# Performance work log

Measured on AMD Instinct MI355X. Metric: run time of the kernel, lower is better.

Reference implementation:

```python
import jax, jax.numpy as jnp
import numpy as np

NEG_SLOPE = 0.2  # PyG GATConv default negative_slope


def _gat_conv(h, src, dst, N, W, a_src, a_dst, b, heads):
    """PyG GATConv (eval mode, self-loops already in src/dst).
    h: [N, F_in], W: [F_in, heads*C], a_src/a_dst: [heads, C], b: [heads*C]."""
    C = W.shape[1] // heads
    hl = (h @ W).reshape(N, heads, C)                      # [N,H,C]
    al_s = jnp.einsum('nhc,hc->nh', hl, a_src)             # [N,H]
    al_d = jnp.einsum('nhc,hc->nh', hl, a_dst)             # [N,H]
    e = jax.nn.leaky_relu(al_s[src] + al_d[dst], NEG_SLOPE)  # [E,H]
    # segment softmax over incoming edges of each destination node
    m = jax.ops.segment_max(e, dst, num_segments=N)        # [N,H]
    ex = jnp.exp(e - m[dst])
    s = jax.ops.segment_sum(ex, dst, num_segments=N)
    alpha = ex / (s[dst] + 1e-16)                          # [E,H]
    out = jax.ops.segment_sum(hl[src] * alpha[:, :, None], dst, num_segments=N)
    return out.reshape(N, heads * C) + b


def setup_inputs() -> dict:
    key = jax.random.key(0)
    ks = jax.random.split(key, 16)
    N, E, D = 30000, 240000, 64
    NUM_ENT, NUM_REL, NUM_DRUGS = 100000, 64, 200
    sc = 0.1
    return {
        'x': jax.random.randint(ks[0], (N,), 0, NUM_ENT),
        'edge_index': jax.random.randint(ks[1], (2, E), 0, N),
        'edge_type': jax.random.randint(ks[2], (N,), 0, NUM_REL),
        'ent_emb': jax.random.normal(ks[3], (NUM_ENT, D), jnp.float32) * sc,
        'rel_emb': jax.random.normal(ks[4], (NUM_REL, D), jnp.float32) * sc,
        'W1': jax.random.normal(ks[5], (2 * D, 8 * D), jnp.float32) * sc,
        'att1_src': jax.random.normal(ks[6], (8, D), jnp.float32) * sc,
        'att1_dst': jax.random.normal(ks[7], (8, D), jnp.float32) * sc,
        'b1': jax.random.normal(ks[8], (8 * D,), jnp.float32) * sc,
        'W2': jax.random.normal(ks[9], (9 * D, D), jnp.float32) * sc,
        'att2_src': jax.random.normal(ks[10], (1, D), jnp.float32) * sc,
        'att2_dst': jax.random.normal(ks[11], (1, D), jnp.float32) * sc,
        'b2': jax.random.normal(ks[12], (D,), jnp.float32) * sc,
        'fc_w': jax.random.normal(ks[13], (D, NUM_DRUGS), jnp.float32) * sc,
        'fc_b': jax.random.normal(ks[14], (NUM_DRUGS,), jnp.float32) * sc,
    }


def reference(x, edge_index, edge_type, ent_emb, rel_emb, W1, att1_src, att1_dst, b1,
              W2, att2_src, att2_dst, b2, fc_w, fc_b):
    N = x.shape[0]
    loop = jnp.arange(N)
    src = jnp.concatenate([edge_index[0], loop])  # GATConv add_self_loops=True
    dst = jnp.concatenate([edge_index[1], loop])
    ent = ent_emb[x]                               # [N,D]
    rel = rel_emb[edge_type]                       # [N,D]
    h = jnp.concatenate([ent, rel], axis=-1)       # [N,2D]  (dropout is identity in eval)
    h = jax.nn.elu(_gat_conv(h, src, dst, N, W1, att1_src, att1_dst, b1, heads=8))  # [N,8D]
    h = jnp.concatenate([h, ent], axis=-1)         # [N,9D]
    h = jax.nn.elu(_gat_conv(h, src, dst, N, W2, att2_src, att2_dst, b2, heads=1))  # [N,D]
    g = jnp.mean(h, axis=0, keepdims=True)         # [1,D]
    return g @ fc_w + fc_b                         # [1,num_drugs]
```

## Files before the change

### kernel.cpp

```cpp
#include <hip/hip_runtime.h>
#include <math.h>

#define NEG_SLOPE 0.2f

typedef __attribute__((ext_vector_type(8))) short short8;
typedef __attribute__((ext_vector_type(4))) float f32x4;
typedef __attribute__((ext_vector_type(2))) float f32x2;

__device__ __forceinline__ float lrelu(float v) { return v > 0.f ? v : NEG_SLOPE * v; }
__device__ __forceinline__ float elu(float v) { return v > 0.f ? v : (__expf(v) - 1.f); }
__device__ __forceinline__ unsigned short f2b(float f) {
    unsigned u = __float_as_uint(f);
    return (unsigned short)((u + 0x7FFFu + ((u >> 16) & 1u)) >> 16);
}
__device__ __forceinline__ unsigned packb(float a, float b) {
    return ((unsigned)f2b(b) << 16) | (unsigned)f2b(a);
}
__device__ __forceinline__ unsigned short pack8(float a, float b) {
    return (unsigned short)(__builtin_amdgcn_cvt_pk_fp8_f32(a, b, 0, false) & 0xFFFF);
}
__device__ __forceinline__ f32x2 unpack8(unsigned v) {
    return __builtin_amdgcn_cvt_pk_f32_fp8((int)v, false);
}
__device__ __forceinline__ f32x2 unpack8hi(unsigned v) {
    return __builtin_amdgcn_cvt_pk_f32_fp8((int)v, true);
}
__device__ __forceinline__ unsigned bpack_trunc(f32x2 f) {
    return (__float_as_uint(f.y) & 0xFFFF0000u) | (__float_as_uint(f.x) >> 16);
}
__device__ __forceinline__ int sw(int r, int o) { return (o ^ (r & 7)) << 3; }

__global__ void prep_k(const int* __restrict__ x, const int* __restrict__ et,
                       const int* __restrict__ ei,
                       const float* __restrict__ ent_emb, const float* __restrict__ rel_emb,
                       const float* __restrict__ W1, const float* __restrict__ W2,
                       unsigned* __restrict__ h1b2, unsigned short* __restrict__ W1t,
                       unsigned short* __restrict__ W2t, unsigned char* __restrict__ h2q8,
                       int* __restrict__ deg, int N, int E) {
    int t = blockIdx.x * blockDim.x + threadIdx.x;
    if (t < N * 64) {
        int n = t >> 6, j = t & 63;
        float v0, v1;
        if (j < 32) {
            const float* e = ent_emb + (size_t)x[n] * 64 + 2 * j;
            v0 = e[0]; v1 = e[1];
            *(unsigned short*)(h2q8 + (size_t)n * 576 + 512 + 2 * j) = pack8(v0, v1);
        } else {
            const float* r = rel_emb + (size_t)et[n] * 64 + 2 * (j - 32);
            v0 = r[0]; v1 = r[1];
        }
        h1b2[t] = packb(v0, v1);
    }
    if (t < 512 * 128) {
        int n = t >> 7, kk = t & 127;
        W1t[t] = f2b(W1[(size_t)kk * 512 + n]);
    }
    if (t < 64 * 576) {
        int n = t / 576, k = t % 576;
        W2t[t] = f2b(W2[(size_t)k * 64 + n]);
    }
    if (t < E + N) {
        int dst = t < E ? ei[E + t] : t - E;
        atomicAdd(&deg[dst], 1);
    }
}

__global__ __launch_bounds__(256) void scan_k(const int* __restrict__ deg,
                                              int* __restrict__ offs,
                                              int* __restrict__ bstate,
                                              int N, int Etot, int NB) {
    __shared__ int s[256];
    __shared__ int sbase;
    int b = blockIdx.x, t = threadIdx.x;
    int i = b * 256 + t;
    int v = (i < N) ? deg[i] : 0;
    s[t] = v;
    __syncthreads();
    for (int off = 1; off < 256; off <<= 1) {
        int tmp = (t >= off) ? s[t - off] : 0;
        __syncthreads();
        s[t] += tmp;
        __syncthreads();
    }
    int total = s[255];
    if (t == 0) {
        if (b == 0) {
            atomicExch(&bstate[0], (total << 2) | 2);
            sbase = 0;
        } else {
            atomicExch(&bstate[b], (total << 2) | 1);
            int run = 0;
            for (int p = b - 1; p >= 0;) {
                int stv;
                do { stv = atomicAdd(&bstate[p], 0); } while ((stv & 3) == 0);
                run += (stv >> 2);
                if ((stv & 3) == 2) break;
                p--;
            }
            atomicExch(&bstate[b], ((run + total) << 2) | 2);
            sbase = run;
        }
    }
    __syncthreads();
    if (i < N) offs[i] = sbase + s[t] - v;
    if (b == NB - 1 && t == 0) offs[N] = Etot;
}

__global__ __launch_bounds__(256) void fillgemm1_k(const int* __restrict__ ei, int E, int N,
                                                   const int* __restrict__ offs,
                                                   int* __restrict__ cursor,
                                                   int* __restrict__ csr,
                                                   const unsigned short* __restrict__ A,
                                                   const unsigned short* __restrict__ W1t,
                                                   const float* __restrict__ a1s,
                                                   const float* __restrict__ a1d,
                                                   unsigned char* __restrict__ hl8,
                                                   float* __restrict__ als,
                                                   float* __restrict__ ald,
                                                   int FB, int NMB) {
    __shared__ __align__(16) unsigned short As[128 * 128];
    __shared__ __align__(16) unsigned short Bs[64 * 128];
    int bid = blockIdx.x;
    int tid = threadIdx.x;
    if (bid < FB) {
        int e = bid * 256 + tid;
        if (e < E + N) {
            int src = e < E ? ei[e] : e - E;
            int dst = e < E ? ei[E + e] : e - E;
            int pos = offs[dst] + atomicAdd(&cursor[dst], 1);
            csr[pos] = src;
        }
        return;
    }
    int g = bid - FB;
    int h = g / NMB, mb = g - h * NMB;
    int m0 = mb * 128;
    int M = N;
    for (int c = tid; c < 2048; c += 256) {
        int r = c >> 4, o = c & 15;
        int gr = m0 + r;
        uint4 v = make_uint4(0u, 0u, 0u, 0u);
        if (gr < M) v = *(const uint4*)(A + (size_t)gr * 128 + o * 8);
        *(uint4*)(As + r * 128 + sw(r, o)) = v;
    }
    for (int c = tid; c < 1024; c += 256) {
        int r = c >> 4, o = c & 15;
        uint4 v = *(const uint4*)(W1t + (size_t)(h * 64 + r) * 128 + o * 8);
        *(uint4*)(Bs + r * 128 + sw(r, o)) = v;
    }
    __syncthreads();
    int w = tid >> 6, lane = tid & 63;
    int wr = w * 32;
    int m16 = lane & 15, quad = lane >> 4;
    f32x4 acc[2][4] = {};
#pragma unroll
    for (int kk = 0; kk < 128; kk += 32) {
        int ob = (kk >> 3) + quad;
        short8 b[4];
#pragma unroll
        for (int j = 0; j < 4; j++) {
            int r = j * 16 + m16;
            b[j] = *(const short8*)(Bs + r * 128 + sw(r, ob));
        }
#pragma unroll
        for (int i = 0; i < 2; i++) {
            int r = wr + i * 16 + m16;
            short8 a = *(const short8*)(As + r * 128 + sw(r, ob));
#pragma unroll
            for (int j = 0; j < 4; j++)
                acc[i][j] = __builtin_amdgcn_mfma_f32_16x16x32_bf16(a, b[j], acc[i][j], 0, 0, 0);
        }
    }
#pragma unroll
    for (int i = 0; i < 2; i++)
#pragma unroll
        for (int j = 0; j < 4; j++)
#pragma unroll
            for (int reg = 0; reg < 4; reg++) {
                int row = m0 + wr + i * 16 + quad * 4 + reg;
                int col = h * 64 + j * 16 + m16;
                if (row < M)
                    hl8[(size_t)row * 512 + col] =
                        (unsigned char)(__builtin_amdgcn_cvt_pk_fp8_f32(acc[i][j][reg] * 8.f,
                                                                        0.f, 0, false) & 0xFF);
            }
    float sa[2][4] = {}, sd[2][4] = {};
#pragma unroll
    for (int j = 0; j < 4; j++) {
        int col = h * 64 + j * 16 + m16;
        float ws_ = a1s[col], wd_ = a1d[col];
#pragma unroll
        for (int i = 0; i < 2; i++)
#pragma unroll
            for (int reg = 0; reg < 4; reg++) {
                sa[i][reg] += acc[i][j][reg] * ws_;
                sd[i][reg] += acc[i][j][reg] * wd_;
            }
    }
#pragma unroll
    for (int m = 1; m < 16; m <<= 1)
#pragma unroll
        for (int i = 0; i < 2; i++)
#pragma unroll
            for (int reg = 0; reg < 4; reg++) {
                sa[i][reg] += __shfl_xor(sa[i][reg], m, 64);
                sd[i][reg] += __shfl_xor(sd[i][reg], m, 64);
            }
    if (m16 == 0)
#pragma unroll
        for (int i = 0; i < 2; i++)
#pragma unroll
            for (int reg = 0; reg < 4; reg++) {
                int row = m0 + wr + i * 16 + quad * 4 + reg;
                if (row < M) { als[row * 8 + h] = sa[i][reg]; ald[row * 8 + h] = sd[i][reg]; }
            }
}

#define ACCP(e_, u_)                                      \
    {                                                     \
        f32x2 g0 = unpack8(u_.x), g1 = unpack8hi(u_.x);   \
        f32x2 g2 = unpack8(u_.y), g3 = unpack8hi(u_.y);   \
        acc[0] += (e_) * g0.x; acc[1] += (e_) * g0.y;     \
        acc[2] += (e_) * g1.x; acc[3] += (e_) * g1.y;     \
        acc[4] += (e_) * g2.x; acc[5] += (e_) * g2.y;     \
        acc[6] += (e_) * g3.x; acc[7] += (e_) * g3.y;     \
    }

__global__ __launch_bounds__(256) void agg1_k(const unsigned char* __restrict__ hl8,
                                              const float* __restrict__ als1,
                                              const float* __restrict__ ald1,
                                              const float* __restrict__ b1,
                                              const int* __restrict__ offs,
                                              const int* __restrict__ csr,
                                              unsigned char* __restrict__ h2q8, int N) {
    int wv = threadIdx.x >> 6;
    int t = threadIdx.x & 63;
    int n = blockIdx.x * 4 + wv;
    if (n >= N) return;
    int h = t >> 3;
    float dl = ald1[n * 8 + h];
    int p0 = offs[n], p1 = offs[n + 1];
    float acc[8] = {};
    float ssum = 0.f;
    int p = p0;
    for (; p + 4 <= p1; p += 4) {
        int sA = csr[p], sB = csr[p + 1], sC = csr[p + 2], sD = csr[p + 3];
        float eA = __expf(lrelu(als1[sA * 8 + h] + dl));
        float eB = __expf(lrelu(als1[sB * 8 + h] + dl));
        float eC = __expf(lrelu(als1[sC * 8 + h] + dl));
        float eD = __expf(lrelu(als1[sD * 8 + h] + dl));
        uint2 vA = *(const uint2*)(hl8 + (size_t)sA * 512 + t * 8);
        uint2 vB = *(const uint2*)(hl8 + (size_t)sB * 512 + t * 8);
        uint2 vC = *(const uint2*)(hl8 + (size_t)sC * 512 + t * 8);
        uint2 vD = *(const uint2*)(hl8 + (size_t)sD * 512 + t * 8);
        ssum += (eA + eB) + (eC + eD);
        ACCP(eA, vA);
        ACCP(eB, vB);
        ACCP(eC, vC);
        ACCP(eD, vD);
    }
    for (; p < p1; p++) {
        int sA = csr[p];
        float eA = __expf(lrelu(als1[sA * 8 + h] + dl));
        uint2 vA = *(const uint2*)(hl8 + (size_t)sA * 512 + t * 8);
        ssum += eA;
        ACCP(eA, vA);
    }
    float iv = 0.125f / (ssum + 1e-16f);
    float4 bq0 = *(const float4*)(b1 + t * 8);
    float4 bq1 = *(const float4*)(b1 + t * 8 + 4);
    float r0 = elu(acc[0] * iv + bq0.x);
    float r1 = elu(acc[1] * iv + bq0.y);
    float r2 = elu(acc[2] * iv + bq0.z);
    float r3 = elu(acc[3] * iv + bq0.w);
    float r4 = elu(acc[4] * iv + bq1.x);
    float r5 = elu(acc[5] * iv + bq1.y);
    float r6 = elu(acc[6] * iv + bq1.z);
    float r7 = elu(acc[7] * iv + bq1.w);
    uint2 o;
    int d0 = __builtin_amdgcn_cvt_pk_fp8_f32(r0, r1, 0, false);
    o.x = (unsigned)__builtin_amdgcn_cvt_pk_fp8_f32(r2, r3, d0, true);
    int d1 = __builtin_amdgcn_cvt_pk_fp8_f32(r4, r5, 0, false);
    o.y = (unsigned)__builtin_amdgcn_cvt_pk_fp8_f32(r6, r7, d1, true);
    *(uint2*)(h2q8 + (size_t)n * 576 + t * 8) = o;
}

__global__ __launch_bounds__(256) void gemm2_k(const unsigned char* __restrict__ Aq8,
                                               const unsigned short* __restrict__ Bt,
                                               const float* __restrict__ a2s,
                                               const float* __restrict__ a2d,
                                               unsigned char* __restrict__ hl2q,
                                               float* __restrict__ als2,
                                               float* __restrict__ ald2, int M) {
    __shared__ __align__(16) unsigned short As[64 * 64];
    __shared__ __align__(16) unsigned short Bs[64 * 64];
    int tid = threadIdx.x;
    int m0 = blockIdx.x * 64;
    int w = tid >> 6, lane = tid & 63;
    int m16 = lane & 15, quad = lane >> 4;
    f32x4 acc[4] = {};
    for (int k0 = 0; k0 < 576; k0 += 64) {
        __syncthreads();
        {
            int r = tid >> 2, o = tid & 3;
            int gr = m0 + r;
            uint4 v = make_uint4(0u, 0u, 0u, 0u);
            if (gr < M) v = *(const uint4*)(Aq8 + (size_t)gr * 576 + k0 + o * 16);
            uint4 w0, w1;
            w0.x = bpack_trunc(unpack8(v.x));   w0.y = bpack_trunc(unpack8hi(v.x));
            w0.z = bpack_trunc(unpack8(v.y));   w0.w = bpack_trunc(unpack8hi(v.y));
            w1.x = bpack_trunc(unpack8(v.z));   w1.y = bpack_trunc(unpack8hi(v.z));
            w1.z = bpack_trunc(unpack8(v.w));   w1.w = bpack_trunc(unpack8hi(v.w));
            *(uint4*)(As + r * 64 + sw(r, 2 * o)) = w0;
            *(uint4*)(As + r * 64 + sw(r, 2 * o + 1)) = w1;
        }
        for (int c = tid; c < 512; c += 256) {
            int r = c >> 3, o = c & 7;
            uint4 v = *(const uint4*)(Bt + (size_t)r * 576 + k0 + o * 8);
            *(uint4*)(Bs + r * 64 + sw(r, o)) = v;
        }
        __syncthreads();
#pragma unroll
        for (int kk = 0; kk < 64; kk += 32) {
            int ob = (kk >> 3) + quad;
            int r = w * 16 + m16;
            short8 a = *(const short8*)(As + r * 64 + sw(r, ob));
#pragma unroll
            for (int j = 0; j < 4; j++) {
                int rb = j * 16 + m16;
                short8 b = *(const short8*)(Bs + rb * 64 + sw(rb, ob));
                acc[j] = __builtin_amdgcn_mfma_f32_16x16x32_bf16(a, b, acc[j], 0, 0, 0);
            }
        }
    }
#pragma unroll
    for (int j = 0; j < 4; j++)
#pragma unroll
        for (int reg = 0; reg < 4; reg++) {
            int row = m0 + w * 16 + quad * 4 + reg;
            int col = j * 16 + m16;
            if (row < M)
                hl2q[(size_t)row * 64 + col] =
                    (unsigned char)(__builtin_amdgcn_cvt_pk_fp8_f32(acc[j][reg], 0.f, 0, false) & 0xFF);
        }
    float sa[4] = {}, sd[4] = {};
#pragma unroll
    for (int j = 0; j < 4; j++) {
        int col = j * 16 + m16;
        float as_ = a2s[col], ad_ = a2d[col];
#pragma unroll
        for (int reg = 0; reg < 4; reg++) {
            sa[reg] += acc[j][reg] * as_;
            sd[reg] += acc[j][reg] * ad_;
        }
    }
#pragma unroll
    for (int m = 1; m < 16; m <<= 1)
#pragma unroll
        for (int reg = 0; reg < 4; reg++) {
            sa[reg] += __shfl_xor(sa[reg], m, 64);
            sd[reg] += __shfl_xor(sd[reg], m, 64);
        }
    if (m16 == 0)
#pragma unroll
        for (int reg = 0; reg < 4; reg++) {
            int row = m0 + w * 16 + quad * 4 + reg;
            if (row < M) { als2[row] = sa[reg]; ald2[row] = sd[reg]; }
        }
}

__global__ __launch_bounds__(256) void agg2_k(const unsigned short* __restrict__ hl2q16,
                                              const float* __restrict__ als2,
                                              const float* __restrict__ ald2,
                                              const float* __restrict__ b2,
                                              const int* __restrict__ offs,
                                              const int* __restrict__ csr,
                                              float* __restrict__ gpart, int N) {
    __shared__ float red[512];
    int slot = threadIdx.x >> 5, l = threadIdx.x & 31;
    int n = blockIdx.x * 8 + slot;
    float v0 = 0.f, v1 = 0.f;
    if (n < N) {
        float dl = ald2[n];
        int p0 = offs[n], p1 = offs[n + 1];
        float a0 = 0.f, a1 = 0.f, ssum = 0.f;
        int p = p0;
        for (; p + 1 < p1; p += 2) {
            int sA = csr[p], sB = csr[p + 1];
            float lA = als2[sA], lB = als2[sB];
            unsigned hA = hl2q16[sA * 32 + l];
            unsigned hB = hl2q16[sB * 32 + l];
            float xA = __expf(lrelu(lA + dl));
            float xB = __expf(lrelu(lB + dl));
            ssum += xA + xB;
            f32x2 fA = unpack8(hA), fB = unpack8(hB);
            a0 += xA * fA.x + xB * fB.x;
            a1 += xA * fA.y + xB * fB.y;
        }
        if (p < p1) {
            int sA = csr[p];
            float xA = __expf(lrelu(als2[sA] + dl));
            ssum += xA;
            f32x2 fA = unpack8(hl2q16[sA * 32 + l]);
            a0 += xA * fA.x;
            a1 += xA * fA.y;
        }
        float inv = 1.f / (ssum + 1e-16f);
        v0 = elu(a0 * inv + b2[2 * l]);
        v1 = elu(a1 * inv + b2[2 * l + 1]);
    }
    red[slot * 64 + 2 * l] = v0;
    red[slot * 64 + 2 * l + 1] = v1;
    __syncthreads();
    if (threadIdx.x < 64) {
        float s = 0.f;
#pragma unroll
        for (int ss = 0; ss < 8; ss++) s += red[ss * 64 + threadIdx.x];
        gpart[(size_t)blockIdx.x * 64 + threadIdx.x] = s;
    }
}

__global__ __launch_bounds__(256) void colredfinal_k(const float* __restrict__ gpart,
                                                     float* __restrict__ gsum,
                                                     int* __restrict__ done,
                                                     const float* __restrict__ fcw,
                                                     const float* __restrict__ fcb,
                                                     float* __restrict__ out,
                                                     int NBL, int N, int NCB) {
    __shared__ float red[256];
    __shared__ int isLast;
    int t = threadIdx.x;
    int c = t & 63, rg = t >> 6;
    int bend = blockIdx.x * 256 + 256; if (bend > NBL) bend = NBL;
    float acc = 0.f;
    for (int b = blockIdx.x * 256 + rg; b < bend; b += 4)
        acc += gpart[(size_t)b * 64 + c];
    red[t] = acc;
    __syncthreads();
    if (t < 64) atomicAdd(&gsum[c], red[c] + red[c + 64] + red[c + 128] + red[c + 192]);
    __threadfence();
    if (t == 0) {
        int old = atomicAdd(done, 1);
        isLast = (old == NCB - 1) ? 1 : 0;
    }
    __syncthreads();
    if (isLast) {
        __shared__ float g[64];
        if (t < 64) g[t] = atomicAdd(&gsum[t], 0.f) / (float)N;
        __syncthreads();
        if (t < 200) {
            float a = fcb[t];
#pragma unroll
            for (int cc = 0; cc < 64; cc++) a += g[cc] * fcw[cc * 200 + t];
            out[t] = a;
        }
    }
}

extern "C" void kernel_launch(void* const* d_in, const int* in_sizes, int n_in,
                              void* d_out, int out_size, void* d_ws, size_t ws_size,
                              hipStream_t stream) {
    const int* x = (const int*)d_in[0];
    const int* ei = (const int*)d_in[1];
    const int* et = (const int*)d_in[2];
    const float* ent_emb = (const float*)d_in[3];
    const float* rel_emb = (const float*)d_in[4];
    const float* W1 = (const float*)d_in[5];
    const float* a1s = (const float*)d_in[6];
    const float* a1d = (const float*)d_in[7];
    const float* b1 = (const float*)d_in[8];
    const float* W2 = (const float*)d_in[9];
    const float* a2s = (const float*)d_in[10];
    const float* a2d = (const float*)d_in[11];
    const float* b2 = (const float*)d_in[12];
    const float* fcw = (const float*)d_in[13];
    const float* fcb = (const float*)d_in[14];
    float* out = (float*)d_out;

    int N = in_sizes[0];
    int E = in_sizes[1] / 2;
    int Etot = E + N;
    int NB = (N + 255) / 256;
    int NBL = (N + 7) / 8;
    int NCB = (NBL + 255) / 256;
    int FB = (Etot + 255) / 256;
    int NMB = (N + 127) / 128;

    char* p = (char*)d_ws;
    auto alloc = [&](size_t bytes) -> char* {
        char* r = p;
        p += (bytes + 255) & ~(size_t)255;
        return r;
    };
    unsigned* h1b2 = (unsigned*)alloc((size_t)N * 64 * 4);
    unsigned short* W1t = (unsigned short*)alloc((size_t)512 * 128 * 2);
    unsigned short* W2t = (unsigned short*)alloc((size_t)64 * 576 * 2);
    float* als1 = (float*)alloc((size_t)N * 8 * 4);
    float* ald1 = (float*)alloc((size_t)N * 8 * 4);
    unsigned char* hl8 = (unsigned char*)alloc((size_t)N * 512);
    unsigned char* h2q8 = (unsigned char*)alloc((size_t)N * 576);
    unsigned char* hl2q = (unsigned char*)alloc((size_t)N * 64);
    float* als2 = (float*)alloc((size_t)N * 4);
    float* ald2 = (float*)alloc((size_t)N * 4);
    float* gpart = (float*)alloc((size_t)NBL * 64 * 4);
    int* offs   = (int*)alloc((size_t)(N + 1) * 4);
    int* csr    = (int*)alloc((size_t)Etot * 4);
    char* z0 = p;
    int* deg    = (int*)alloc((size_t)N * 4);
    int* cursor = (int*)alloc((size_t)N * 4);
    float* gsum = (float*)alloc(64 * 4);
    int* done   = (int*)alloc(4);
    int* bstate = (int*)alloc((size_t)NB * 4);
    size_t zbytes = (size_t)(p - z0);

    int tb = 256;
    hipMemsetAsync(z0, 0, zbytes, stream);
    prep_k<<<(N * 64 + tb - 1) / tb, tb, 0, stream>>>(x, et, ei, ent_emb, rel_emb,
                                                      W1, W2, h1b2, W1t, W2t, h2q8, deg, N, E);
    scan_k<<<NB, 256, 0, stream>>>(deg, offs, bstate, N, Etot, NB);
    fillgemm1_k<<<FB + NMB * 8, 256, 0, stream>>>(ei, E, N, offs, cursor, csr,
                                                  (const unsigned short*)h1b2, W1t,
                                                  a1s, a1d, hl8, als1, ald1, FB, NMB);
    agg1_k<<<(N + 3) / 4, 256, 0, stream>>>(hl8, als1, ald1, b1, offs, csr, h2q8, N);
    gemm2_k<<<(N + 63) / 64, 256, 0, stream>>>(h2q8, W2t, a2s, a2d, hl2q, als2, ald2, N);
    agg2_k<<<NBL, 256, 0, stream>>>((const unsigned short*)hl2q, als2, ald2, b2, offs, csr, gpart, N);
    colredfinal_k<<<NCB, 256, 0, stream>>>(gpart, gsum, done, fcw, fcb, out, NBL, N, NCB);
}
```

Baseline: 234.5 us.

## Load GEMM operands directly from global and stage fp8 output through LDS

The GEMM part of the fused fill/gemm kernel stops staging A and W1t tiles in shared memory. Each MFMA operand fragment is now read straight from global memory, which drops the LDS fill and its barrier and shrinks shared memory from 48KB to 8KB, allowing higher occupancy. The fp8 output, previously written as scattered single bytes, is now gathered in a small LDS tile and written out as coalesced 16-byte stores. The trade-off is more global/L2 traffic from redundant operand reads across waves, and a new barrier before the store.

```diff
diff --git a/kernel.cpp b/kernel.cpp
--- a/kernel.cpp
+++ b/kernel.cpp
@@ -118,8 +118,7 @@
                                                    float* __restrict__ als,
                                                    float* __restrict__ ald,
                                                    int FB, int NMB) {
-    __shared__ __align__(16) unsigned short As[128 * 128];
-    __shared__ __align__(16) unsigned short Bs[64 * 128];
+    __shared__ __align__(16) unsigned char Cs[128 * 64];
     int bid = blockIdx.x;
     int tid = threadIdx.x;
     if (bid < FB) {
@@ -136,54 +135,27 @@
     int h = g / NMB, mb = g - h * NMB;
     int m0 = mb * 128;
     int M = N;
-    for (int c = tid; c < 2048; c += 256) {
-        int r = c >> 4, o = c & 15;
-        int gr = m0 + r;
-        uint4 v = make_uint4(0u, 0u, 0u, 0u);
-        if (gr < M) v = *(const uint4*)(A + (size_t)gr * 128 + o * 8);
-        *(uint4*)(As + r * 128 + sw(r, o)) = v;
-    }
-    for (int c = tid; c < 1024; c += 256) {
-        int r = c >> 4, o = c & 15;
-        uint4 v = *(const uint4*)(W1t + (size_t)(h * 64 + r) * 128 + o * 8);
-        *(uint4*)(Bs + r * 128 + sw(r, o)) = v;
-    }
-    __syncthreads();
     int w = tid >> 6, lane = tid & 63;
     int wr = w * 32;
     int m16 = lane & 15, quad = lane >> 4;
     f32x4 acc[2][4] = {};
 #pragma unroll
     for (int kk = 0; kk < 128; kk += 32) {
-        int ob = (kk >> 3) + quad;
+        int col = kk + quad * 8;
         short8 b[4];
 #pragma unroll
-        for (int j = 0; j < 4; j++) {
-            int r = j * 16 + m16;
-            b[j] = *(const short8*)(Bs + r * 128 + sw(r, ob));
-        }
+        for (int j = 0; j < 4; j++)
+            b[j] = *(const short8*)(W1t + (size_t)(h * 64 + j * 16 + m16) * 128 + col);
 #pragma unroll
         for (int i = 0; i < 2; i++) {
-            int r = wr + i * 16 + m16;
-            short8 a = *(const short8*)(As + r * 128 + sw(r, ob));
+            int r = m0 + wr + i * 16 + m16;
+            short8 a = {};
+            if (r < M) a = *(const short8*)(A + (size_t)r * 128 + col);
 #pragma unroll
             for (int j = 0; j < 4; j++)
                 acc[i][j] = __builtin_amdgcn_mfma_f32_16x16x32_bf16(a, b[j], acc[i][j], 0, 0, 0);
         }
     }
-#pragma unroll
-    for (int i = 0; i < 2; i++)
-#pragma unroll
-        for (int j = 0; j < 4; j++)
-#pragma unroll
-            for (int reg = 0; reg < 4; reg++) {
-                int row = m0 + wr + i * 16 + quad * 4 + reg;
-                int col = h * 64 + j * 16 + m16;
-                if (row < M)
-                    hl8[(size_t)row * 512 + col] =
-                        (unsigned char)(__builtin_amdgcn_cvt_pk_fp8_f32(acc[i][j][reg] * 8.f,
-                                                                        0.f, 0, false) & 0xFF);
-            }
     float sa[2][4] = {}, sd[2][4] = {};
 #pragma unroll
     for (int j = 0; j < 4; j++) {
@@ -214,6 +186,25 @@
                 int row = m0 + wr + i * 16 + quad * 4 + reg;
                 if (row < M) { als[row * 8 + h] = sa[i][reg]; ald[row * 8 + h] = sd[i][reg]; }
             }
+#pragma unroll
+    for (int i = 0; i < 2; i++)
+#pragma unroll
+        for (int j = 0; j < 4; j++)
+#pragma unroll
+            for (int reg = 0; reg < 4; reg++) {
+                int lr = wr + i * 16 + quad * 4 + reg;
+                Cs[lr * 64 + j * 16 + m16] =
+                    (unsigned char)(__builtin_amdgcn_cvt_pk_fp8_f32(acc[i][j][reg] * 8.f,
+                                                                    0.f, 0, false) & 0xFF);
+            }
+    __syncthreads();
+    for (int c = tid; c < 512; c += 256) {
+        int row = c >> 2, off = c & 3;
+        int grow = m0 + row;
+        if (grow < M)
+            *(uint4*)(hl8 + (size_t)grow * 512 + h * 64 + off * 16) =
+                *(const uint4*)(Cs + c * 16);
+    }
 }
 
 #define ACCP(e_, u_)                                      \
```

New measurement: 238.4 us. No clear change (+1.7%).
